# Kernel optimization log

Measured on AMD Instinct MI355X. Metric: run time of the kernel, lower is better.

The kernel has to match this reference:

```python
import jax, jax.numpy as jnp
import numpy as np

TOPK = 9
NUM_CLASSES = 80
BG_INDEX = NUM_CLASSES
B, N_GT = 16, 32
N_LEVEL_BBOXES = (25600, 6400, 1600)  # strides 8/16/32 on a 1280x1280 image
M = sum(N_LEVEL_BBOXES)
EPS = 1e-9


def _make_boxes(key, lead_shape, img_size=1280.0):
    k1, k2 = jax.random.split(key)
    c = jax.random.uniform(k1, lead_shape + (2,), minval=32.0, maxval=img_size - 32.0)
    wh = jax.random.uniform(k2, lead_shape + (2,), minval=8.0, maxval=256.0)
    return jnp.concatenate([c - wh * 0.5, c + wh * 0.5], axis=-1)


def setup_inputs() -> dict:
    key = jax.random.key(0)
    ks = jax.random.split(key, 5)
    anchor_bboxes = _make_boxes(ks[0], (M,))
    gt_bboxes = _make_boxes(ks[1], (B, N_GT))
    gt_labels = jax.random.randint(ks[2], (B, N_GT, 1), 0, NUM_CLASSES)
    mask_gt = (jax.random.uniform(ks[3], (B, N_GT, 1)) < 0.8).astype(jnp.float32)
    pred_bboxes = _make_boxes(ks[4], (B, M))
    return {"anchor_bboxes": anchor_bboxes, "n_level_bboxes": N_LEVEL_BBOXES,
            "gt_bboxes": gt_bboxes, "gt_labels": gt_labels,
            "mask_gt": mask_gt, "pred_bboxes": pred_bboxes}


def pairwise_iou(box1, box2):
    # box1 [..., N, 4], box2 [..., M, 4] -> [..., N, M]
    b1 = box1[..., :, None, :]
    b2 = box2[..., None, :, :]
    lt = jnp.maximum(b1[..., :2], b2[..., :2])
    rb = jnp.minimum(b1[..., 2:], b2[..., 2:])
    inter = jnp.clip(rb - lt, 0.0).prod(-1)
    area1 = (b1[..., 2:] - b1[..., :2]).prod(-1)
    area2 = (b2[..., 2:] - b2[..., :2]).prod(-1)
    return inter / (area1 + area2 - inter + EPS)


def reference(anchor_bboxes, n_level_bboxes, gt_bboxes, gt_labels, mask_gt, pred_bboxes):
    bs, n_max = gt_bboxes.shape[0], gt_bboxes.shape[1]
    n_anchors = anchor_bboxes.shape[0]

    overlaps = pairwise_iou(gt_bboxes.reshape(-1, 4), anchor_bboxes).reshape(bs, n_max, n_anchors)
    gt_centers = (gt_bboxes[..., :2] + gt_bboxes[..., 2:]) * 0.5            # [B,N,2]
    anchor_points = (anchor_bboxes[:, :2] + anchor_bboxes[:, 2:]) * 0.5      # [M,2]
    distances = jnp.sqrt(((gt_centers[:, :, None, :] - anchor_points[None, None, :, :]) ** 2).sum(-1))
    distances = jax.lax.stop_gradient(distances)  # only feeds integer topk indices

    # ---- per-FPN-level topk candidate selection (dedup via scatter-count) ----
    mask_gt_b = mask_gt.astype(bool)                 # [B,N,1]
    b_ix = jnp.arange(bs)[:, None, None]
    n_ix = jnp.arange(n_max)[None, :, None]
    is_in_candidate_list, candidate_indices = [], []
    start = 0
    for L in n_level_bboxes:
        k = min(TOPK, L)
        d = jax.lax.dynamic_slice_in_dim(distances, start, L, axis=-1)
        _, idx = jax.lax.top_k(-d, k)                # [B,N,k] k smallest distances
        candidate_indices.append(idx + start)
        idx_m = jnp.where(mask_gt_b, idx, 0)
        cnt = jnp.zeros((bs, n_max, L), distances.dtype).at[b_ix, n_ix, idx_m].add(1.0)
        cnt = jnp.where(cnt > 1, 0.0, cnt)           # drop duplicated indices
        is_in_candidate_list.append(cnt)
        start += L
    is_in_candidate = jnp.concatenate(is_in_candidate_list, -1)   # [B,N,M]
    candidate_indices = jnp.concatenate(candidate_indices, -1)    # [B,N,k*l]

    # ---- dynamic IoU threshold = mean + std over candidate overlaps ----
    iou_candidates = jnp.where(is_in_candidate > 0, overlaps, 0.0)
    gathered = jnp.take_along_axis(iou_candidates, candidate_indices, axis=-1)
    thr = gathered.mean(-1, keepdims=True) + gathered.std(-1, keepdims=True, ddof=1)
    is_positive = jnp.where(iou_candidates > thr, is_in_candidate, 0.0)

    # ---- anchor centers strictly inside gt boxes ----
    deltas = jnp.concatenate([anchor_points[None, None] - gt_bboxes[:, :, None, :2],
                              gt_bboxes[:, :, None, 2:] - anchor_points[None, None]], -1)
    is_in_gts = (deltas.min(-1) > EPS).astype(overlaps.dtype)     # [B,N,M]

    mask_positive = is_positive * is_in_gts * mask_gt

    # ---- resolve anchors matched to multiple gts by highest overlap ----
    fg_mask = mask_positive.sum(-2)                               # [B,M]
    multi = fg_mask[:, None, :] > 1
    is_max = jax.nn.one_hot(overlaps.argmax(1), n_max, dtype=mask_positive.dtype).transpose(0, 2, 1)
    mask_positive = jnp.where(multi, is_max, mask_positive)
    fg_mask = mask_positive.sum(-2)
    target_gt_index = mask_positive.argmax(-2)                    # [B,M]

    # ---- gather targets ----
    target_labels = jnp.take_along_axis(gt_labels[..., 0], target_gt_index, axis=1)
    target_labels = jnp.where(fg_mask > 0, target_labels, BG_INDEX)
    target_bboxes = jnp.take_along_axis(gt_bboxes, target_gt_index[..., None], axis=1)  # [B,M,4]
    target_scores = jax.nn.one_hot(target_labels, NUM_CLASSES + 1, dtype=jnp.float32)[..., :NUM_CLASSES]

    # ---- soft-label scaling by predicted-box IoU ----
    ious = pairwise_iou(gt_bboxes, pred_bboxes) * mask_positive
    target_scores = target_scores * ious.max(-2)[..., None]
    return target_labels, target_bboxes, target_scores, fg_mask > 0
```

## Files before the change

kernel.cpp:

```cpp
#include <hip/hip_runtime.h>
#include <stdint.h>

#define NCLS 80
#define BGI 80
#define BB 16
#define NGT 32
#define MM 33600
#define EPSF 1e-9f
#define CAP 1024
#define ZPB 21000

__device__ __forceinline__ float iou_f(const float4 b1, const float4 b2) {
#pragma clang fp contract(off)
  float ltx = fmaxf(b1.x, b2.x);
  float lty = fmaxf(b1.y, b2.y);
  float rbx = fminf(b1.z, b2.z);
  float rby = fminf(b1.w, b2.w);
  float iw = fmaxf(rbx - ltx, 0.0f);
  float ih = fmaxf(rby - lty, 0.0f);
  float inter = iw * ih;
  float a1 = (b1.z - b1.x) * (b1.w - b1.y);
  float a2 = (b2.z - b2.x) * (b2.w - b2.y);
  return inter / (a1 + a2 - inter + EPSF);
}

__global__ __launch_bounds__(256) void k_prep(
    const float4* __restrict__ anchors, float2* __restrict__ centers,
    unsigned int* __restrict__ pk) {
#pragma clang fp contract(off)
  const int i = blockIdx.x * 256 + threadIdx.x;
  if (i < MM) {
    const float4 ab = anchors[i];
    centers[i] = make_float2((ab.x + ab.z) * 0.5f, (ab.y + ab.w) * 0.5f);
  }
  pk[i] = 0u;
}

__global__ __launch_bounds__(1024) void k_topk(
    const float4* __restrict__ anchors, const float2* __restrict__ centers,
    const float4* __restrict__ gtb, const float* __restrict__ maskgt,
    unsigned int* __restrict__ pk, float4* __restrict__ zscores) {
#pragma clang fp contract(off)
  const int tid = threadIdx.x;
  const int bid = (int)blockIdx.x;

  if ((bid >> 8) & 1) {
    const int zb = (bid & 255) | ((bid >> 9) << 8);
    float4* z = zscores + (size_t)zb * ZPB;
    const float4 zero4 = make_float4(0.f, 0.f, 0.f, 0.f);
#pragma unroll
    for (int it = 0; it < 21; ++it) {
      const int idx = it * 1024 + tid;
      if (idx < ZPB) z[idx] = zero4;
    }
    return;
  }

  const int pair = (bid & 255) | ((bid >> 9) << 8);
  if (maskgt[pair] == 0.0f) return;
  const int b = pair >> 5;
  const int g = pair & 31;
  const int lane = tid & 63;
  const int wid = tid >> 6;
  const float4 gb = gtb[pair];
  const float gcx = (gb.x + gb.z) * 0.5f;
  const float gcy = (gb.y + gb.w) * 0.5f;

  __shared__ unsigned long long buf[CAP];
  __shared__ unsigned long long winners[27];
  __shared__ float s_wmin[16];
  __shared__ float s_T;
  __shared__ unsigned int s_cnt;

  const int LSTART[3] = {0, 25600, 32000};
  const int LLEN[3]   = {25600, 6400, 1600};

#pragma unroll
  for (int lev = 0; lev < 3; ++lev) {
    const int start = LSTART[lev];
    const int len2 = LLEN[lev] >> 1;
    const float4* c4 = (const float4*)(centers + start);

    float mymin = 3.4e38f;
    for (int p = tid; p < len2; p += 1024) {
      const float4 two = c4[p];
      const float dx0 = gcx - two.x, dy0 = gcy - two.y;
      const float dx1 = gcx - two.z, dy1 = gcy - two.w;
      mymin = fminf(mymin,
                    fminf(dx0 * dx0 + dy0 * dy0, dx1 * dx1 + dy1 * dy1));
    }
#pragma unroll
    for (int s = 32; s >= 1; s >>= 1)
      mymin = fminf(mymin, __shfl_xor(mymin, s, 64));
    if (lane == 0) s_wmin[wid] = mymin;
    if (tid == 0) s_cnt = 0u;
    __syncthreads();

    if (wid == 0 && lane < 16) {
      const float v = s_wmin[lane];
      int r = 0;
#pragma unroll
      for (int q = 0; q < 16; ++q) {
        const float o = s_wmin[q];
        r += (o < v) || (o == v && q < lane);
      }
      if (r == 8) s_T = sqrtf(v);
    }
    __syncthreads();
    const float T = s_T;

    for (int p = tid; p < len2; p += 1024) {
      const float4 two = c4[p];
      const float dx0 = gcx - two.x, dy0 = gcy - two.y;
      const float dx1 = gcx - two.z, dy1 = gcy - two.w;
      const float dist0 = sqrtf(dx0 * dx0 + dy0 * dy0);
      const float dist1 = sqrtf(dx1 * dx1 + dy1 * dy1);
      if (dist0 <= T) {
        const unsigned int q = atomicAdd(&s_cnt, 1u);
        if (q < CAP)
          buf[q] = ((unsigned long long)__float_as_uint(dist0) << 32) |
                   (unsigned long long)(unsigned int)(start + 2 * p);
      }
      if (dist1 <= T) {
        const unsigned int q = atomicAdd(&s_cnt, 1u);
        if (q < CAP)
          buf[q] = ((unsigned long long)__float_as_uint(dist1) << 32) |
                   (unsigned long long)(unsigned int)(start + 2 * p + 1);
      }
    }
    __syncthreads();

    const int m = (int)min(s_cnt, (unsigned int)CAP);
    for (int i = tid; i < m; i += 1024) {
      const unsigned long long k = buf[i];
      int r = 0;
      for (int q = 0; q < m; ++q) r += (buf[q] < k);
      if (r < 9) winners[lev * 9 + r] = k;
    }
    __syncthreads();
  }

  if (wid != 0) return;

  unsigned int mycand = 0;
  if (lane < 27) mycand = (unsigned int)(winners[lane] & 0xffffffffu);

  float ov = 0.0f;
  bool inside = false;
  if (lane < 27) {
    const float4 ab = anchors[mycand];
    ov = iou_f(gb, ab);
    const float2 ac = centers[mycand];
    const float m1 = fminf(fminf(ac.x - gb.x, ac.y - gb.y),
                           fminf(gb.z - ac.x, gb.w - ac.y));
    inside = m1 > EPSF;
  }
  float s = (lane < 27) ? ov : 0.0f;
#pragma unroll
  for (int sft = 32; sft >= 1; sft >>= 1) s += __shfl_xor(s, sft, 64);
  const float mean = s / 27.0f;
  float dev = (lane < 27) ? (ov - mean) : 0.0f;
  float s2 = dev * dev;
#pragma unroll
  for (int sft = 32; sft >= 1; sft >>= 1) s2 += __shfl_xor(s2, sft, 64);
  const float thr = mean + sqrtf(s2 / 26.0f);

  if (lane < 27 && inside && ov > thr) {
    atomicAdd(&pk[b * MM + (int)mycand], (1u << 20) | (unsigned int)g);
  }
}

__global__ __launch_bounds__(256) void k_out(
    const float4* __restrict__ anchors, const float4* __restrict__ gtb,
    const int* __restrict__ glabels, const float4* __restrict__ predb,
    const unsigned int* __restrict__ pk,
    float* __restrict__ out_labels, float4* __restrict__ out_bbox,
    float* __restrict__ out_fg, float* __restrict__ out_scores) {
  const int a = blockIdx.x * 256 + threadIdx.x;
  if (a >= MM) return;
  const int b = blockIdx.y;
  const int i = b * MM + a;
  const unsigned int p = pk[i];
  const unsigned int c = p >> 20;
  int g = 0;
  const bool fg = (c != 0u);
  if (c == 1u) {
    g = (int)(p & 0xFFFFFu);
  } else if (c > 1u) {
    const float4 ab = anchors[a];
    float best = -1.0f;
    for (int gg = 0; gg < NGT; ++gg) {
      const float ovv = iou_f(gtb[b * NGT + gg], ab);
      if (ovv > best) { best = ovv; g = gg; }
    }
  }
  const int lbl = fg ? glabels[b * NGT + g] : BGI;
  out_labels[i] = (float)lbl;
  out_bbox[i] = gtb[b * NGT + g];
  out_fg[i] = fg ? 1.0f : 0.0f;
  if (fg) {
    const float io = iou_f(gtb[b * NGT + g], predb[i]);
    out_scores[(size_t)i * NCLS + lbl] = io;
  }
}

extern "C" void kernel_launch(void* const* d_in, const int* in_sizes, int n_in,
                              void* d_out, int out_size, void* d_ws, size_t ws_size,
                              hipStream_t stream) {
  const float* anchors = nullptr;
  const float* gtb = nullptr;
  const int* glab = nullptr;
  const float* maskgt = nullptr;
  const float* predb = nullptr;
  int seen512 = 0;
  for (int i = 0; i < n_in; ++i) {
    const int sz = in_sizes[i];
    if (sz == 134400 && !anchors) anchors = (const float*)d_in[i];
    else if (sz == 2048 && !gtb) gtb = (const float*)d_in[i];
    else if (sz == 512) {
      if (seen512++ == 0) glab = (const int*)d_in[i];
      else maskgt = (const float*)d_in[i];
    } else if (sz == 2150400 && !predb) predb = (const float*)d_in[i];
  }
  if (!anchors || !gtb || !glab || !maskgt || !predb) return;

  float* out = (float*)d_out;
  float* out_labels = out;
  float4* out_bbox = (float4*)(out + 537600);
  float* out_scores = out + 2688000;
  float* out_fg = out + 45696000;

  unsigned int* pk = (unsigned int*)d_ws;
  float2* centers = (float2*)(pk + 537600);

  k_prep<<<dim3(2100), dim3(256), 0, stream>>>(
      (const float4*)anchors, centers, pk);

  k_topk<<<dim3(1024), dim3(1024), 0, stream>>>(
      (const float4*)anchors, centers, (const float4*)gtb, maskgt, pk,
      (float4*)out_scores);

  k_out<<<dim3(132, BB), dim3(256), 0, stream>>>(
      (const float4*)anchors, (const float4*)gtb, glab, (const float4*)predb,
      pk, out_labels, out_bbox, out_fg, out_scores);
}
```

Baseline: 54.08 us.

## Split per-gt topk scan across chunk blocks with global candidate buffers

The per-(batch,gt) topk kernel, which had one 1024-thread block scan all three FPN levels, is split into many 256-thread blocks. Each block handles one 3200-anchor chunk, computes a local 9th-smallest distance threshold and appends candidates to a per-level global buffer through global atomics. A new small kernel then ranks the candidates per level, runs the mean+std IoU selection, and writes the positive-mask counters. Zeroing of the score output is spread over more, smaller blocks. This aims to raise parallelism and avoid the two full passes over the centers. It adds an extra launch, global atomic contention, and a 256-entry candidate cap that could overflow.

```diff
diff --git a/kernel.cpp b/kernel.cpp
--- a/kernel.cpp
+++ b/kernel.cpp
@@ -7,8 +7,10 @@
 #define NGT 32
 #define MM 33600
 #define EPSF 1e-9f
-#define CAP 1024
-#define ZPB 21000
+#define CAPL 256
+#define NSCAN 5632
+#define NZ4 10752000
+#define ZPB 1910
 
 __device__ __forceinline__ float iou_f(const float4 b1, const float4 b2) {
 #pragma clang fp contract(off)
@@ -26,7 +28,7 @@
 
 __global__ __launch_bounds__(256) void k_prep(
     const float4* __restrict__ anchors, float2* __restrict__ centers,
-    unsigned int* __restrict__ pk) {
+    unsigned int* __restrict__ pk, unsigned int* __restrict__ cc) {
 #pragma clang fp contract(off)
   const int i = blockIdx.x * 256 + threadIdx.x;
   if (i < MM) {
@@ -34,113 +36,133 @@
     centers[i] = make_float2((ab.x + ab.z) * 0.5f, (ab.y + ab.w) * 0.5f);
   }
   pk[i] = 0u;
-}
-
-__global__ __launch_bounds__(1024) void k_topk(
+  if (i < 512 * 3) cc[i] = 0u;
+}
+
+__global__ __launch_bounds__(256) void k_main(
+    const float2* __restrict__ centers, const float4* __restrict__ gtb,
+    const float* __restrict__ maskgt, unsigned int* __restrict__ cc,
+    unsigned long long* __restrict__ cand, float4* __restrict__ zscores) {
+#pragma clang fp contract(off)
+  const int tid = threadIdx.x;
+  const int bid = (int)blockIdx.x;
+  const int sid = (bid & 255) | ((bid >> 9) << 8);
+
+  if ((bid >> 8) & 1) {
+    const float4 zero4 = make_float4(0.f, 0.f, 0.f, 0.f);
+    const int base = sid * ZPB;
+#pragma unroll
+    for (int it = 0; it < 8; ++it) {
+      const int idx = it * 256 + tid;
+      const int g2 = base + idx;
+      if (idx < ZPB && g2 < NZ4) zscores[g2] = zero4;
+    }
+    return;
+  }
+
+  const int pair = sid / 11;
+  const int c = sid - pair * 11;
+  if (maskgt[pair] == 0.0f) return;
+
+  int lev, start, len4;
+  if (c < 8)       { lev = 0; start = c * 3200;              len4 = 1600; }
+  else if (c < 10) { lev = 1; start = 25600 + (c - 8) * 3200; len4 = 1600; }
+  else             { lev = 2; start = 32000;                 len4 = 800;  }
+
+  const float4 gb = gtb[pair];
+  const float gcx = (gb.x + gb.z) * 0.5f;
+  const float gcy = (gb.y + gb.w) * 0.5f;
+  const float4* c4 = (const float4*)centers + (start >> 1);
+
+  __shared__ float s_gmin[16];
+
+  float dd0[7], dd1[7];
+  float gm = 3.4e38f;
+#pragma unroll
+  for (int it = 0; it < 7; ++it) {
+    const int p = it * 256 + tid;
+    float d0 = 3.4e38f, d1 = 3.4e38f;
+    if (p < len4) {
+      const float4 two = c4[p];
+      const float dx0 = gcx - two.x, dy0 = gcy - two.y;
+      const float dx1 = gcx - two.z, dy1 = gcy - two.w;
+      d0 = sqrtf(dx0 * dx0 + dy0 * dy0);
+      d1 = sqrtf(dx1 * dx1 + dy1 * dy1);
+    }
+    dd0[it] = d0;
+    dd1[it] = d1;
+    gm = fminf(gm, fminf(d0, d1));
+  }
+#pragma unroll
+  for (int s = 8; s >= 1; s >>= 1)
+    gm = fminf(gm, __shfl_xor(gm, s, 64));
+  if ((tid & 15) == 0) s_gmin[tid >> 4] = gm;
+  __syncthreads();
+
+  float T = 0.0f;
+#pragma unroll
+  for (int cw = 0; cw < 16; ++cw) {
+    const float v = s_gmin[cw];
+    int r = 0;
+#pragma unroll
+    for (int q = 0; q < 16; ++q) {
+      const float o = s_gmin[q];
+      r += (o < v) || (o == v && q < cw);
+    }
+    if (r == 8) T = v;
+  }
+
+  unsigned int* myc = &cc[pair * 3 + lev];
+  unsigned long long* mybuf = cand + (size_t)(pair * 3 + lev) * CAPL;
+#pragma unroll
+  for (int it = 0; it < 7; ++it) {
+    const int p = it * 256 + tid;
+    if (dd0[it] <= T) {
+      const unsigned int slot = atomicAdd(myc, 1u);
+      if (slot < CAPL)
+        mybuf[slot] = ((unsigned long long)__float_as_uint(dd0[it]) << 32) |
+                      (unsigned long long)(unsigned int)(start + 2 * p);
+    }
+    if (dd1[it] <= T) {
+      const unsigned int slot = atomicAdd(myc, 1u);
+      if (slot < CAPL)
+        mybuf[slot] = ((unsigned long long)__float_as_uint(dd1[it]) << 32) |
+                      (unsigned long long)(unsigned int)(start + 2 * p + 1);
+    }
+  }
+}
+
+__global__ __launch_bounds__(64) void k_sel(
     const float4* __restrict__ anchors, const float2* __restrict__ centers,
     const float4* __restrict__ gtb, const float* __restrict__ maskgt,
-    unsigned int* __restrict__ pk, float4* __restrict__ zscores) {
-#pragma clang fp contract(off)
-  const int tid = threadIdx.x;
-  const int bid = (int)blockIdx.x;
-
-  if ((bid >> 8) & 1) {
-    const int zb = (bid & 255) | ((bid >> 9) << 8);
-    float4* z = zscores + (size_t)zb * ZPB;
-    const float4 zero4 = make_float4(0.f, 0.f, 0.f, 0.f);
-#pragma unroll
-    for (int it = 0; it < 21; ++it) {
-      const int idx = it * 1024 + tid;
-      if (idx < ZPB) z[idx] = zero4;
-    }
-    return;
-  }
-
-  const int pair = (bid & 255) | ((bid >> 9) << 8);
+    const unsigned int* __restrict__ cc,
+    const unsigned long long* __restrict__ cand,
+    unsigned int* __restrict__ pk) {
+#pragma clang fp contract(off)
+  const int pair = blockIdx.x;
   if (maskgt[pair] == 0.0f) return;
   const int b = pair >> 5;
   const int g = pair & 31;
-  const int lane = tid & 63;
-  const int wid = tid >> 6;
+  const int lane = threadIdx.x;
   const float4 gb = gtb[pair];
-  const float gcx = (gb.x + gb.z) * 0.5f;
-  const float gcy = (gb.y + gb.w) * 0.5f;
-
-  __shared__ unsigned long long buf[CAP];
+
+  __shared__ unsigned long long keys[CAPL];
   __shared__ unsigned long long winners[27];
-  __shared__ float s_wmin[16];
-  __shared__ float s_T;
-  __shared__ unsigned int s_cnt;
-
-  const int LSTART[3] = {0, 25600, 32000};
-  const int LLEN[3]   = {25600, 6400, 1600};
 
 #pragma unroll
   for (int lev = 0; lev < 3; ++lev) {
-    const int start = LSTART[lev];
-    const int len2 = LLEN[lev] >> 1;
-    const float4* c4 = (const float4*)(centers + start);
-
-    float mymin = 3.4e38f;
-    for (int p = tid; p < len2; p += 1024) {
-      const float4 two = c4[p];
-      const float dx0 = gcx - two.x, dy0 = gcy - two.y;
-      const float dx1 = gcx - two.z, dy1 = gcy - two.w;
-      mymin = fminf(mymin,
-                    fminf(dx0 * dx0 + dy0 * dy0, dx1 * dx1 + dy1 * dy1));
-    }
-#pragma unroll
-    for (int s = 32; s >= 1; s >>= 1)
-      mymin = fminf(mymin, __shfl_xor(mymin, s, 64));
-    if (lane == 0) s_wmin[wid] = mymin;
-    if (tid == 0) s_cnt = 0u;
+    const int m = (int)min(cc[pair * 3 + lev], (unsigned int)CAPL);
+    const unsigned long long* src = cand + (size_t)(pair * 3 + lev) * CAPL;
+    for (int i = lane; i < m; i += 64) keys[i] = src[i];
     __syncthreads();
-
-    if (wid == 0 && lane < 16) {
-      const float v = s_wmin[lane];
+    for (int i = lane; i < m; i += 64) {
+      const unsigned long long k = keys[i];
       int r = 0;
-#pragma unroll
-      for (int q = 0; q < 16; ++q) {
-        const float o = s_wmin[q];
-        r += (o < v) || (o == v && q < lane);
-      }
-      if (r == 8) s_T = sqrtf(v);
+      for (int q = 0; q < m; ++q) r += (keys[q] < k);
+      if (r < 9) winners[lev * 9 + r] = k;
     }
     __syncthreads();
-    const float T = s_T;
-
-    for (int p = tid; p < len2; p += 1024) {
-      const float4 two = c4[p];
-      const float dx0 = gcx - two.x, dy0 = gcy - two.y;
-      const float dx1 = gcx - two.z, dy1 = gcy - two.w;
-      const float dist0 = sqrtf(dx0 * dx0 + dy0 * dy0);
-      const float dist1 = sqrtf(dx1 * dx1 + dy1 * dy1);
-      if (dist0 <= T) {
-        const unsigned int q = atomicAdd(&s_cnt, 1u);
-        if (q < CAP)
-          buf[q] = ((unsigned long long)__float_as_uint(dist0) << 32) |
-                   (unsigned long long)(unsigned int)(start + 2 * p);
-      }
-      if (dist1 <= T) {
-        const unsigned int q = atomicAdd(&s_cnt, 1u);
-        if (q < CAP)
-          buf[q] = ((unsigned long long)__float_as_uint(dist1) << 32) |
-                   (unsigned long long)(unsigned int)(start + 2 * p + 1);
-      }
-    }
-    __syncthreads();
-
-    const int m = (int)min(s_cnt, (unsigned int)CAP);
-    for (int i = tid; i < m; i += 1024) {
-      const unsigned long long k = buf[i];
-      int r = 0;
-      for (int q = 0; q < m; ++q) r += (buf[q] < k);
-      if (r < 9) winners[lev * 9 + r] = k;
-    }
-    __syncthreads();
-  }
-
-  if (wid != 0) return;
+  }
 
   unsigned int mycand = 0;
   if (lane < 27) mycand = (unsigned int)(winners[lane] & 0xffffffffu);
@@ -232,13 +254,19 @@
 
   unsigned int* pk = (unsigned int*)d_ws;
   float2* centers = (float2*)(pk + 537600);
+  unsigned int* cc = (unsigned int*)(centers + MM);
+  unsigned long long* cand =
+      (unsigned long long*)(cc + 512 * 3);
 
   k_prep<<<dim3(2100), dim3(256), 0, stream>>>(
-      (const float4*)anchors, centers, pk);
-
-  k_topk<<<dim3(1024), dim3(1024), 0, stream>>>(
-      (const float4*)anchors, centers, (const float4*)gtb, maskgt, pk,
-      (float4*)out_scores);
+      (const float4*)anchors, centers, pk, cc);
+
+  k_main<<<dim3(2 * NSCAN), dim3(256), 0, stream>>>(
+      centers, (const float4*)gtb, maskgt, cc, cand, (float4*)out_scores);
+
+  k_sel<<<dim3(512), dim3(64), 0, stream>>>(
+      (const float4*)anchors, centers, (const float4*)gtb, maskgt, cc, cand,
+      pk);
 
   k_out<<<dim3(132, BB), dim3(256), 0, stream>>>(
       (const float4*)anchors, (const float4*)gtb, glab, (const float4*)predb,
```

Result: slower. 88.08 us (+62.9%).
